# Kernel optimization log

Hardware: AMD Instinct MI355X
Metric: run time of the kernel (lower is better)

Reference implementation:

```python
import jax, jax.numpy as jnp
import numpy as np

NUM_QUBITS = 4
NUM_LAYERS = 3


def _ry(state, theta, wire):
    # state: (N,2,2,2,2) real amplitudes; RY(theta) on `wire` (angle scalar or (N,))
    st = jnp.moveaxis(state, wire + 1, -1)
    c = jnp.cos(theta * 0.5)
    s = jnp.sin(theta * 0.5)
    if jnp.ndim(c) == 1:  # per-sample angle -> broadcast over remaining qubit axes
        shape = (c.shape[0],) + (1,) * (st.ndim - 2)
        c = c.reshape(shape)
        s = s.reshape(shape)
    s0, s1 = st[..., 0], st[..., 1]
    new = jnp.stack([c * s0 - s * s1, s * s0 + c * s1], axis=-1)
    return jnp.moveaxis(new, -1, wire + 1)


def _cnot(state, control, target):
    st = jnp.moveaxis(state, (control + 1, target + 1), (-2, -1))
    new = jnp.stack([st[..., 0, :], st[..., 1, ::-1]], axis=-2)
    return jnp.moveaxis(new, (-2, -1), (control + 1, target + 1))


def _circuit(angles, params):
    # angles: (N,4) input rotations; params: (L,4,1) shared variational angles
    N = angles.shape[0]
    state = jnp.zeros((N, 2, 2, 2, 2), angles.dtype).at[:, 0, 0, 0, 0].set(1.0)
    for q in range(NUM_QUBITS):
        state = _ry(state, angles[:, q], q)
    for l in range(NUM_LAYERS):
        for q in range(NUM_QUBITS):
            state = _ry(state, params[l, q, 0], q)
        for q in range(NUM_QUBITS - 1):
            state = _cnot(state, q, q + 1)
    probs = state * state  # amplitudes are real (only RY/CNOT)
    meas = []
    for w in range(NUM_QUBITS):
        axes = tuple(a for a in range(1, NUM_QUBITS + 1) if a != w + 1)
        p = probs.sum(axes)  # (N,2)
        meas.append(p[:, 0] - p[:, 1])  # <Z_w>
    return jnp.stack(meas, axis=-1)  # (N,4)


def setup_inputs() -> dict:
    key = jax.random.key(0)
    k1, k2, k3, k4, k5 = jax.random.split(key, 5)
    B = 8192
    return {
        "x": jax.random.uniform(k1, (B, 1, 28, 28), dtype=jnp.float32),
        "params": jax.random.normal(k2, (NUM_LAYERS, NUM_QUBITS, 1), dtype=jnp.float32),
        "res_w": jax.random.normal(k3, (4, 1, 1, 1), dtype=jnp.float32),
        "cls_w": jax.random.normal(k4, (10, 784), dtype=jnp.float32) * 0.03,
        "cls_b": jax.random.normal(k5, (10,), dtype=jnp.float32) * 0.03,
    }


def reference(x, params, res_w, cls_w, cls_b):
    B = x.shape[0]
    img = x.reshape(B, 28, 28)
    # extract 2x2 patches, element order (r,c),(r,c+1),(r+1,c),(r+1,c+1)
    patches = img.reshape(B, 14, 2, 14, 2).transpose(0, 1, 3, 2, 4).reshape(B, 196, 4)
    # per-patch-index min/max over batch and the 4 elements (matches patch.min()/max())
    mn = patches.min(axis=(0, 2), keepdims=True)
    mx = patches.max(axis=(0, 2), keepdims=True)
    ang = (patches - mn) / (mx - mn + 1e-8) * jnp.pi
    meas = _circuit(ang.reshape(B * 196, 4), params)  # (B*196, 4)
    out = meas.reshape(B, 196 * 4).reshape(B, 4, 14, 14)  # matches torch.cat(...).view
    # res_conv: 1x1 conv, stride 2, no bias -> strided pixel scaled per out-channel
    res = img[:, ::2, ::2][:, None, :, :] * res_w.reshape(1, 4, 1, 1)
    out = out + res
    logits = out.reshape(B, -1) @ cls_w.T + cls_b
    return jax.nn.log_softmax(logits, axis=-1)
```

## Files before the change

### kernel.cpp

```cpp
#include <hip/hip_runtime.h>
#include <math.h>

#define NP 196
#define PI_F 3.14159265358979323846f

__device__ __forceinline__ unsigned fkey(float f) {
  unsigned u = __float_as_uint(f);
  return u ^ ((unsigned)((int)u >> 31) | 0x80000000u);
}
__device__ __forceinline__ float funkey(unsigned k) {
  unsigned u = (k & 0x80000000u) ? (k ^ 0x80000000u) : ~k;
  return __uint_as_float(u);
}

__global__ void __launch_bounds__(256) precompute_kernel(
    const float* __restrict__ params, const float* __restrict__ res_w,
    const float* __restrict__ cls_w, float* __restrict__ U,
    float* __restrict__ W2) {
  const int tid = threadIdx.x;
  if (tid < 16) {
    float cp[12], sp[12];
#pragma unroll
    for (int l = 0; l < 12; ++l) __sincosf(0.5f * params[l], &sp[l], &cp[l]);
    float st[16];
#pragma unroll
    for (int i = 0; i < 16; ++i) st[i] = 0.f;
    st[tid] = 1.f;
#pragma unroll
    for (int l = 0; l < 3; ++l) {
#pragma unroll
      for (int q = 0; q < 4; ++q) {
        const float cq = cp[l * 4 + q], sq = sp[l * 4 + q];
        const int m = 8 >> q;
#pragma unroll
        for (int idx = 0; idx < 16; ++idx) {
          if (idx & m) continue;
          float v0 = st[idx], v1 = st[idx | m];
          st[idx] = cq * v0 - sq * v1;
          st[idx | m] = sq * v0 + cq * v1;
        }
      }
#pragma unroll
      for (int q = 0; q < 3; ++q) {
        const int mc = 8 >> q, mt = 4 >> q;
#pragma unroll
        for (int idx = 0; idx < 16; ++idx) {
          if ((idx & mc) && !(idx & mt)) {
            float t0 = st[idx];
            st[idx] = st[idx | mt];
            st[idx | mt] = t0;
          }
        }
      }
    }
#pragma unroll
    for (int i = 0; i < 16; ++i) U[i * 16 + tid] = st[i];
  }
  for (int t = tid; t < 10 * NP; t += 256) {
    int k = t / NP, p = t - k * NP;
    float s = 0.f;
#pragma unroll
    for (int c = 0; c < 4; ++c) s += res_w[c] * cls_w[k * 784 + c * NP + p];
    W2[t] = s;
  }
}

__global__ void __launch_bounds__(512) minmax_kernel(
    const float* __restrict__ x, unsigned* __restrict__ mn,
    unsigned* __restrict__ mx, int imgs, int B) {
  __shared__ unsigned skmin[392], skmax[392];
  const int t = threadIdx.x;
  const int img0 = blockIdx.x * imgs;
  if (t < 392) {
    const int r = t / 14, j = t - r * 14;
    const float* base = x + (size_t)img0 * 784 + r * 28 + 2 * j;
    float lmn = 3.4e38f, lmx = -3.4e38f;
    const int nimg = (img0 + imgs <= B) ? imgs : (B - img0);
#pragma unroll 4
    for (int m = 0; m < nimg; ++m) {
      float2 v = *(const float2*)(base + (size_t)m * 784);
      lmn = fminf(lmn, fminf(v.x, v.y));
      lmx = fmaxf(lmx, fmaxf(v.x, v.y));
    }
    skmin[t] = fkey(lmn);
    skmax[t] = fkey(lmx);
  }
  __syncthreads();
  if (t < NP) {
    const int i = t / 14, j = t - i * 14;
    const int f0 = (2 * i) * 14 + j, f1 = f0 + 14;
    unsigned kmn = skmin[f0] < skmin[f1] ? skmin[f0] : skmin[f1];
    unsigned kmx = skmax[f0] > skmax[f1] ? skmax[f0] : skmax[f1];
    atomicMin(&mn[t], kmn);
    atomicMax(&mx[t], kmx);
  }
}

__global__ void __launch_bounds__(256) circuit_kernel(
    const float* __restrict__ x, const unsigned* __restrict__ mnk,
    const unsigned* __restrict__ mxk, const float* __restrict__ U,
    float4* __restrict__ gmeas, int G) {
  const int g = blockIdx.x * 256 + threadIdx.x;
  if (g >= G) return;
  const int b = g / NP;
  const int p = g - b * NP;
  const int i = p / 14, j = p - i * 14;

  const float* px = x + (size_t)b * 784 + (2 * i) * 28 + 2 * j;
  const float2 r0 = *(const float2*)px;
  const float2 r1 = *(const float2*)(px + 28);

  const float mnv = funkey(mnk[p]);
  const float mxv = funkey(mxk[p]);
  const float sc = (0.5f * PI_F) / (mxv - mnv + 1e-8f);

  float cc[4], ss[4];
  __sincosf((r0.x - mnv) * sc, &ss[0], &cc[0]);
  __sincosf((r0.y - mnv) * sc, &ss[1], &cc[1]);
  __sincosf((r1.x - mnv) * sc, &ss[2], &cc[2]);
  __sincosf((r1.y - mnv) * sc, &ss[3], &cc[3]);

  float st0[16];
  {
    const float A[4] = {cc[0] * cc[1], cc[0] * ss[1], ss[0] * cc[1], ss[0] * ss[1]};
    const float Bq[4] = {cc[2] * cc[3], cc[2] * ss[3], ss[2] * cc[3], ss[2] * ss[3]};
#pragma unroll
    for (int idx = 0; idx < 16; ++idx) st0[idx] = A[idx >> 2] * Bq[idx & 3];
  }

  float z0 = 0.f, z1 = 0.f, z2 = 0.f, z3 = 0.f;
#pragma unroll
  for (int i2 = 0; i2 < 16; ++i2) {
    float f = 0.f;
#pragma unroll
    for (int jx = 0; jx < 16; ++jx) f = fmaf(U[i2 * 16 + jx], st0[jx], f);
    const float sq = f * f;
    z0 += (i2 & 8) ? -sq : sq;
    z1 += (i2 & 4) ? -sq : sq;
    z2 += (i2 & 2) ? -sq : sq;
    z3 += (i2 & 1) ? -sq : sq;
  }
  gmeas[g] = make_float4(z0, z1, z2, z3);
}

__global__ void __launch_bounds__(256) cls_kernel(
    const float* __restrict__ gmeas, const float* __restrict__ x,
    const float* __restrict__ W2, const float* __restrict__ cls_w,
    const float* __restrict__ cls_b, float* __restrict__ out, int B) {
  const int wv = (blockIdx.x * 256 + threadIdx.x) >> 6;
  const int lane = threadIdx.x & 63;
  if (wv >= B) return;
  const float* mrow = gmeas + (size_t)wv * 784;
  const float* xrow = x + (size_t)wv * 784;

  float acc[10];
#pragma unroll
  for (int k = 0; k < 10; ++k) acc[k] = 0.f;

  for (int t = lane; t < 784; t += 64) {
    const float v = mrow[t];
#pragma unroll
    for (int k = 0; k < 10; ++k) acc[k] = fmaf(v, cls_w[k * 784 + t], acc[k]);
  }
  for (int p = lane; p < NP; p += 64) {
    const int i = p / 14, j = p - i * 14;
    const float v = xrow[(2 * i) * 28 + 2 * j];
#pragma unroll
    for (int k = 0; k < 10; ++k) acc[k] = fmaf(v, W2[k * NP + p], acc[k]);
  }
#pragma unroll
  for (int k = 0; k < 10; ++k) {
    float a = acc[k];
#pragma unroll
    for (int off = 32; off > 0; off >>= 1) a += __shfl_down(a, off, 64);
    acc[k] = a;
  }
  if (lane == 0) {
    float lg[10];
#pragma unroll
    for (int k = 0; k < 10; ++k) lg[k] = acc[k] + cls_b[k];
    float m = lg[0];
#pragma unroll
    for (int k = 1; k < 10; ++k) m = fmaxf(m, lg[k]);
    float s = 0.f;
#pragma unroll
    for (int k = 0; k < 10; ++k) s += __expf(lg[k] - m);
    const float lse = m + __logf(s);
#pragma unroll
    for (int k = 0; k < 10; ++k) out[(size_t)wv * 10 + k] = lg[k] - lse;
  }
}

extern "C" void kernel_launch(void* const* d_in, const int* in_sizes, int n_in,
                              void* d_out, int out_size, void* d_ws, size_t ws_size,
                              hipStream_t stream) {
  const float* x      = (const float*)d_in[0];
  const float* params = (const float*)d_in[1];
  const float* res_w  = (const float*)d_in[2];
  const float* cls_w  = (const float*)d_in[3];
  const float* cls_b  = (const float*)d_in[4];
  float* out = (float*)d_out;
  const int B = in_sizes[0] / 784;

  unsigned* mn = (unsigned*)d_ws;
  unsigned* mx = mn + NP;
  float* U  = (float*)(mx + NP);
  float* W2 = U + 256;
  float* gmeas = W2 + 10 * NP;

  hipMemsetAsync(mn, 0xFF, NP * sizeof(unsigned), stream);
  hipMemsetAsync(mx, 0x00, NP * sizeof(unsigned), stream);

  precompute_kernel<<<1, 256, 0, stream>>>(params, res_w, cls_w, U, W2);

  const int imgs = 16;
  const int nblk1 = (B + imgs - 1) / imgs;
  minmax_kernel<<<nblk1, 512, 0, stream>>>(x, mn, mx, imgs, B);

  const int G = B * NP;
  circuit_kernel<<<(G + 255) / 256, 256, 0, stream>>>(x, mn, mx, U, (float4*)gmeas, G);

  cls_kernel<<<(B * 64 + 255) / 256, 256, 0, stream>>>(gmeas, x, W2, cls_w, cls_b, out, B);
}
```

Measured before the change: 130.9 us.

## Fold memsets into precompute, vectorize minmax and cls loads, batch circuit samples per thread

New measurement: 146.5 us. 11.9% more time.

```diff
diff --git a/kernel.cpp b/kernel.cpp
--- a/kernel.cpp
+++ b/kernel.cpp
@@ -3,6 +3,7 @@
 
 #define NP 196
 #define PI_F 3.14159265358979323846f
+#define CS 4
 
 __device__ __forceinline__ unsigned fkey(float f) {
   unsigned u = __float_as_uint(f);
@@ -16,47 +17,51 @@
 __global__ void __launch_bounds__(256) precompute_kernel(
     const float* __restrict__ params, const float* __restrict__ res_w,
     const float* __restrict__ cls_w, float* __restrict__ U,
-    float* __restrict__ W2) {
+    float* __restrict__ W2, unsigned* __restrict__ mn,
+    unsigned* __restrict__ mx) {
   const int tid = threadIdx.x;
-  if (tid < 16) {
-    float cp[12], sp[12];
-#pragma unroll
-    for (int l = 0; l < 12; ++l) __sincosf(0.5f * params[l], &sp[l], &cp[l]);
-    float st[16];
-#pragma unroll
-    for (int i = 0; i < 16; ++i) st[i] = 0.f;
-    st[tid] = 1.f;
-#pragma unroll
-    for (int l = 0; l < 3; ++l) {
-#pragma unroll
-      for (int q = 0; q < 4; ++q) {
-        const float cq = cp[l * 4 + q], sq = sp[l * 4 + q];
-        const int m = 8 >> q;
-#pragma unroll
-        for (int idx = 0; idx < 16; ++idx) {
-          if (idx & m) continue;
-          float v0 = st[idx], v1 = st[idx | m];
-          st[idx] = cq * v0 - sq * v1;
-          st[idx | m] = sq * v0 + cq * v1;
+  if (blockIdx.x == 0) {
+    if (tid < NP) { mn[tid] = 0xFFFFFFFFu; mx[tid] = 0u; }
+    if (tid < 16) {
+      float cp[12], sp[12];
+#pragma unroll
+      for (int l = 0; l < 12; ++l) __sincosf(0.5f * params[l], &sp[l], &cp[l]);
+      float st[16];
+#pragma unroll
+      for (int i = 0; i < 16; ++i) st[i] = 0.f;
+      st[tid] = 1.f;
+#pragma unroll
+      for (int l = 0; l < 3; ++l) {
+#pragma unroll
+        for (int q = 0; q < 4; ++q) {
+          const float cq = cp[l * 4 + q], sq = sp[l * 4 + q];
+          const int m = 8 >> q;
+#pragma unroll
+          for (int idx = 0; idx < 16; ++idx) {
+            if (idx & m) continue;
+            float v0 = st[idx], v1 = st[idx | m];
+            st[idx] = cq * v0 - sq * v1;
+            st[idx | m] = sq * v0 + cq * v1;
+          }
         }
-      }
-#pragma unroll
-      for (int q = 0; q < 3; ++q) {
-        const int mc = 8 >> q, mt = 4 >> q;
-#pragma unroll
-        for (int idx = 0; idx < 16; ++idx) {
-          if ((idx & mc) && !(idx & mt)) {
-            float t0 = st[idx];
-            st[idx] = st[idx | mt];
-            st[idx | mt] = t0;
+#pragma unroll
+        for (int q = 0; q < 3; ++q) {
+          const int mc = 8 >> q, mt = 4 >> q;
+#pragma unroll
+          for (int idx = 0; idx < 16; ++idx) {
+            if ((idx & mc) && !(idx & mt)) {
+              float t0 = st[idx];
+              st[idx] = st[idx | mt];
+              st[idx | mt] = t0;
+            }
           }
         }
       }
-    }
-#pragma unroll
-    for (int i = 0; i < 16; ++i) U[i * 16 + tid] = st[i];
-  }
-  for (int t = tid; t < 10 * NP; t += 256) {
+#pragma unroll
+      for (int i = 0; i < 16; ++i) U[i * 16 + tid] = st[i];
+    }
+  }
+  for (int t = blockIdx.x * 256 + tid; t < 10 * NP; t += 8 * 256) {
     int k = t / NP, p = t - k * NP;
     float s = 0.f;
 #pragma unroll
@@ -65,102 +70,145 @@
   }
 }
 
-__global__ void __launch_bounds__(512) minmax_kernel(
+__global__ void __launch_bounds__(256) minmax_kernel(
     const float* __restrict__ x, unsigned* __restrict__ mn,
     unsigned* __restrict__ mx, int imgs, int B) {
-  __shared__ unsigned skmin[392], skmax[392];
+  __shared__ float pmn[392], pmx[392];
   const int t = threadIdx.x;
   const int img0 = blockIdx.x * imgs;
-  if (t < 392) {
-    const int r = t / 14, j = t - r * 14;
-    const float* base = x + (size_t)img0 * 784 + r * 28 + 2 * j;
-    float lmn = 3.4e38f, lmx = -3.4e38f;
+  if (t < NP) {
+    const float* base = x + (size_t)img0 * 784 + 4 * t;
+    float mn0 = 3.4e38f, mx0 = -3.4e38f, mn1 = 3.4e38f, mx1 = -3.4e38f;
     const int nimg = (img0 + imgs <= B) ? imgs : (B - img0);
 #pragma unroll 4
     for (int m = 0; m < nimg; ++m) {
-      float2 v = *(const float2*)(base + (size_t)m * 784);
-      lmn = fminf(lmn, fminf(v.x, v.y));
-      lmx = fmaxf(lmx, fmaxf(v.x, v.y));
-    }
-    skmin[t] = fkey(lmn);
-    skmax[t] = fkey(lmx);
+      float4 v = *(const float4*)(base + (size_t)m * 784);
+      mn0 = fminf(mn0, fminf(v.x, v.y));
+      mx0 = fmaxf(mx0, fmaxf(v.x, v.y));
+      mn1 = fminf(mn1, fminf(v.z, v.w));
+      mx1 = fmaxf(mx1, fmaxf(v.z, v.w));
+    }
+    const int r = (4 * t) / 28;
+    const int jj = ((4 * t) - 28 * r) >> 1;
+    pmn[r * 14 + jj] = mn0;
+    pmx[r * 14 + jj] = mx0;
+    pmn[r * 14 + jj + 1] = mn1;
+    pmx[r * 14 + jj + 1] = mx1;
   }
   __syncthreads();
   if (t < NP) {
     const int i = t / 14, j = t - i * 14;
     const int f0 = (2 * i) * 14 + j, f1 = f0 + 14;
-    unsigned kmn = skmin[f0] < skmin[f1] ? skmin[f0] : skmin[f1];
-    unsigned kmx = skmax[f0] > skmax[f1] ? skmax[f0] : skmax[f1];
-    atomicMin(&mn[t], kmn);
-    atomicMax(&mx[t], kmx);
+    atomicMin(&mn[t], fkey(fminf(pmn[f0], pmn[f1])));
+    atomicMax(&mx[t], fkey(fmaxf(pmx[f0], pmx[f1])));
   }
 }
 
 __global__ void __launch_bounds__(256) circuit_kernel(
     const float* __restrict__ x, const unsigned* __restrict__ mnk,
-    const unsigned* __restrict__ mxk, const float* __restrict__ U,
+    const unsigned* __restrict__ mxk, const float* __restrict__ Ug,
     float4* __restrict__ gmeas, int G) {
-  const int g = blockIdx.x * 256 + threadIdx.x;
-  if (g >= G) return;
-  const int b = g / NP;
-  const int p = g - b * NP;
-  const int i = p / 14, j = p - i * 14;
-
-  const float* px = x + (size_t)b * 784 + (2 * i) * 28 + 2 * j;
-  const float2 r0 = *(const float2*)px;
-  const float2 r1 = *(const float2*)(px + 28);
-
-  const float mnv = funkey(mnk[p]);
-  const float mxv = funkey(mxk[p]);
-  const float sc = (0.5f * PI_F) / (mxv - mnv + 1e-8f);
-
-  float cc[4], ss[4];
-  __sincosf((r0.x - mnv) * sc, &ss[0], &cc[0]);
-  __sincosf((r0.y - mnv) * sc, &ss[1], &cc[1]);
-  __sincosf((r1.x - mnv) * sc, &ss[2], &cc[2]);
-  __sincosf((r1.y - mnv) * sc, &ss[3], &cc[3]);
-
-  float st0[16];
-  {
+  __shared__ float sU[256];
+  __shared__ float smn[NP], ssc[NP];
+  const int tid = threadIdx.x;
+  sU[tid] = Ug[tid];
+  if (tid < NP) {
+    const float mnv = funkey(mnk[tid]);
+    const float mxv = funkey(mxk[tid]);
+    smn[tid] = mnv;
+    ssc[tid] = (0.5f * PI_F) / (mxv - mnv + 1e-8f);
+  }
+  __syncthreads();
+
+  const int base = blockIdx.x * (256 * CS) + tid;
+  float st[CS][16];
+  int gi[CS];
+#pragma unroll
+  for (int s = 0; s < CS; ++s) {
+    const int g = base + s * 256;
+    gi[s] = g;
+    const int gc = g < G ? g : G - 1;
+    const int b = gc / NP;
+    const int p = gc - b * NP;
+    const int i = p / 14, j = p - i * 14;
+    const float* px = x + (size_t)b * 784 + (2 * i) * 28 + 2 * j;
+    const float2 r0 = *(const float2*)px;
+    const float2 r1 = *(const float2*)(px + 28);
+    const float mnv = smn[p], sc = ssc[p];
+    float cc[4], ss[4];
+    __sincosf((r0.x - mnv) * sc, &ss[0], &cc[0]);
+    __sincosf((r0.y - mnv) * sc, &ss[1], &cc[1]);
+    __sincosf((r1.x - mnv) * sc, &ss[2], &cc[2]);
+    __sincosf((r1.y - mnv) * sc, &ss[3], &cc[3]);
     const float A[4] = {cc[0] * cc[1], cc[0] * ss[1], ss[0] * cc[1], ss[0] * ss[1]};
     const float Bq[4] = {cc[2] * cc[3], cc[2] * ss[3], ss[2] * cc[3], ss[2] * ss[3]};
 #pragma unroll
-    for (int idx = 0; idx < 16; ++idx) st0[idx] = A[idx >> 2] * Bq[idx & 3];
-  }
-
-  float z0 = 0.f, z1 = 0.f, z2 = 0.f, z3 = 0.f;
+    for (int idx = 0; idx < 16; ++idx) st[s][idx] = A[idx >> 2] * Bq[idx & 3];
+  }
+
+  float zz[CS][4];
+#pragma unroll
+  for (int s = 0; s < CS; ++s)
+#pragma unroll
+    for (int w = 0; w < 4; ++w) zz[s][w] = 0.f;
+
 #pragma unroll
   for (int i2 = 0; i2 < 16; ++i2) {
-    float f = 0.f;
-#pragma unroll
-    for (int jx = 0; jx < 16; ++jx) f = fmaf(U[i2 * 16 + jx], st0[jx], f);
-    const float sq = f * f;
-    z0 += (i2 & 8) ? -sq : sq;
-    z1 += (i2 & 4) ? -sq : sq;
-    z2 += (i2 & 2) ? -sq : sq;
-    z3 += (i2 & 1) ? -sq : sq;
-  }
-  gmeas[g] = make_float4(z0, z1, z2, z3);
+    const float4 u0 = *(const float4*)&sU[i2 * 16 + 0];
+    const float4 u1 = *(const float4*)&sU[i2 * 16 + 4];
+    const float4 u2 = *(const float4*)&sU[i2 * 16 + 8];
+    const float4 u3 = *(const float4*)&sU[i2 * 16 + 12];
+#pragma unroll
+    for (int s = 0; s < CS; ++s) {
+      float f = u0.x * st[s][0];
+      f = fmaf(u0.y, st[s][1], f);
+      f = fmaf(u0.z, st[s][2], f);
+      f = fmaf(u0.w, st[s][3], f);
+      f = fmaf(u1.x, st[s][4], f);
+      f = fmaf(u1.y, st[s][5], f);
+      f = fmaf(u1.z, st[s][6], f);
+      f = fmaf(u1.w, st[s][7], f);
+      f = fmaf(u2.x, st[s][8], f);
+      f = fmaf(u2.y, st[s][9], f);
+      f = fmaf(u2.z, st[s][10], f);
+      f = fmaf(u2.w, st[s][11], f);
+      f = fmaf(u3.x, st[s][12], f);
+      f = fmaf(u3.y, st[s][13], f);
+      f = fmaf(u3.z, st[s][14], f);
+      f = fmaf(u3.w, st[s][15], f);
+      const float sq = f * f;
+      zz[s][0] += (i2 & 8) ? -sq : sq;
+      zz[s][1] += (i2 & 4) ? -sq : sq;
+      zz[s][2] += (i2 & 2) ? -sq : sq;
+      zz[s][3] += (i2 & 1) ? -sq : sq;
+    }
+  }
+#pragma unroll
+  for (int s = 0; s < CS; ++s)
+    if (gi[s] < G) gmeas[gi[s]] = make_float4(zz[s][0], zz[s][1], zz[s][2], zz[s][3]);
 }
 
 __global__ void __launch_bounds__(256) cls_kernel(
-    const float* __restrict__ gmeas, const float* __restrict__ x,
-    const float* __restrict__ W2, const float* __restrict__ cls_w,
+    const float4* __restrict__ gmeas, const float* __restrict__ x,
+    const float* __restrict__ W2, const float4* __restrict__ cls_w4,
     const float* __restrict__ cls_b, float* __restrict__ out, int B) {
   const int wv = (blockIdx.x * 256 + threadIdx.x) >> 6;
   const int lane = threadIdx.x & 63;
   if (wv >= B) return;
-  const float* mrow = gmeas + (size_t)wv * 784;
+  const float4* mrow = gmeas + (size_t)wv * NP;
   const float* xrow = x + (size_t)wv * 784;
 
   float acc[10];
 #pragma unroll
   for (int k = 0; k < 10; ++k) acc[k] = 0.f;
 
-  for (int t = lane; t < 784; t += 64) {
-    const float v = mrow[t];
-#pragma unroll
-    for (int k = 0; k < 10; ++k) acc[k] = fmaf(v, cls_w[k * 784 + t], acc[k]);
+  for (int t4 = lane; t4 < NP; t4 += 64) {
+    const float4 v = mrow[t4];
+#pragma unroll
+    for (int k = 0; k < 10; ++k) {
+      const float4 w = cls_w4[k * NP + t4];
+      acc[k] = fmaf(v.x, w.x, fmaf(v.y, w.y, fmaf(v.z, w.z, fmaf(v.w, w.w, acc[k]))));
+    }
   }
   for (int p = lane; p < NP; p += 64) {
     const int i = p / 14, j = p - i * 14;
@@ -208,17 +256,16 @@
   float* W2 = U + 256;
   float* gmeas = W2 + 10 * NP;
 
-  hipMemsetAsync(mn, 0xFF, NP * sizeof(unsigned), stream);
-  hipMemsetAsync(mx, 0x00, NP * sizeof(unsigned), stream);
-
-  precompute_kernel<<<1, 256, 0, stream>>>(params, res_w, cls_w, U, W2);
+  precompute_kernel<<<8, 256, 0, stream>>>(params, res_w, cls_w, U, W2, mn, mx);
 
   const int imgs = 16;
   const int nblk1 = (B + imgs - 1) / imgs;
-  minmax_kernel<<<nblk1, 512, 0, stream>>>(x, mn, mx, imgs, B);
+  minmax_kernel<<<nblk1, 256, 0, stream>>>(x, mn, mx, imgs, B);
 
   const int G = B * NP;
-  circuit_kernel<<<(G + 255) / 256, 256, 0, stream>>>(x, mn, mx, U, (float4*)gmeas, G);
-
-  cls_kernel<<<(B * 64 + 255) / 256, 256, 0, stream>>>(gmeas, x, W2, cls_w, cls_b, out, B);
-}
+  const int nblk2 = (G + 256 * CS - 1) / (256 * CS);
+  circuit_kernel<<<nblk2, 256, 0, stream>>>(x, mn, mx, U, (float4*)gmeas, G);
+
+  cls_kernel<<<(B * 64 + 255) / 256, 256, 0, stream>>>((const float4*)gmeas, x, W2,
+                                                       (const float4*)cls_w, cls_b, out, B);
+}
```
